# Kernel tuning notes

Measured on AMD Instinct MI355X. Metric: run time of the kernel, lower is better.

## Reference

```python
import jax, jax.numpy as jnp
import numpy as np

B, S, D = 1, 2048, 1024
E, F, TOP_K = 8, 2048, 2
LN_EPS = 1e-5


def setup_inputs() -> dict:
    key = jax.random.key(0)
    ks = jax.random.split(key, 8)
    sc_in = 1.0 / np.sqrt(D)
    sc_hid = 1.0 / np.sqrt(F)
    return {
        "x": jax.random.normal(ks[0], (B, S, D), dtype=jnp.float32),
        "Wr": jax.random.normal(ks[1], (D, E), dtype=jnp.float32) * sc_in,
        "br": jnp.zeros((E,), dtype=jnp.float32),
        "W1": jax.random.normal(ks[2], (E, D, F), dtype=jnp.float32) * sc_in,
        "b1": jnp.zeros((E, F), dtype=jnp.float32),
        "W2": jax.random.normal(ks[3], (E, F, D), dtype=jnp.float32) * sc_hid,
        "b2": jnp.zeros((E, D), dtype=jnp.float32),
        "gamma": jnp.ones((D,), dtype=jnp.float32),
        "beta": jnp.zeros((D,), dtype=jnp.float32),
    }


def reference(x, Wr, br, W1, b1, W2, b2, gamma, beta):
    # x: (B, S, D)
    xf = x.reshape(-1, D)  # (T, D), T = B*S
    # Router: softmax over expert logits, then top-k scores/indices.
    probs = jax.nn.softmax(xf @ Wr + br, axis=-1)           # (T, E)
    scores, idx = jax.lax.top_k(probs, TOP_K)               # (T, K)
    # combine[t, e] = sum_k scores[t, k] * [idx[t, k] == e]  (weighted scatter)
    onehot = jax.nn.one_hot(idx, E, dtype=xf.dtype)         # (T, K, E)
    combine = jnp.einsum('tk,tke->te', scores, onehot)      # (T, E)
    # Per-expert FFN, weighted scatter-add combine. Tokens not routed to an
    # expert have combine weight 0 -> identical math to masked gather/scatter.
    out = jnp.zeros_like(xf)
    for e in range(E):  # E is a small static constant
        h = jax.nn.gelu(xf @ W1[e] + b1[e])                 # (T, F)
        out = out + combine[:, e:e + 1] * (h @ W2[e] + b2[e])
    # Residual + LayerNorm (dropout = 0)
    y = x + out.reshape(B, S, D)
    mu = jnp.mean(y, axis=-1, keepdims=True)
    var = jnp.mean(jnp.square(y - mu), axis=-1, keepdims=True)
    return (y - mu) * jax.lax.rsqrt(var + LN_EPS) * gamma + beta
```

## Files before the change

### kernel.cpp

```cpp
#include <hip/hip_runtime.h>

#define T_TOK 2048
#define DDIM  1024
#define EEXP  8
#define FDIM  2048

typedef __attribute__((ext_vector_type(8))) short bf16x8;
typedef __attribute__((ext_vector_type(4))) float f32x4;
typedef __attribute__((ext_vector_type(4))) unsigned short u16x4;

__device__ __forceinline__ unsigned short f2bf(float f) {
  union { float f; unsigned int u; } v; v.f = f;
  unsigned int r = v.u + 0x7FFF + ((v.u >> 16) & 1);
  return (unsigned short)(r >> 16);
}
__device__ __forceinline__ float gelu_tanh(float x) {
  const float c = 0.7978845608028654f;
  float t = c * (x + 0.044715f * x * x * x);
  return 0.5f * x * (1.0f + tanhf(t));
}
__device__ __forceinline__ void gload_lds16(const void* g, void* lds) {
  __builtin_amdgcn_global_load_lds(
      (const __attribute__((address_space(1))) void*)g,
      (__attribute__((address_space(3))) void*)lds, 16, 0, 0);
}

__global__ __launch_bounds__(256)
void router_kernel(const float* __restrict__ x, const float* __restrict__ Wr,
                   const float* __restrict__ br, float* __restrict__ combine) {
  int t = blockIdx.x;
  int tid = threadIdx.x;
  float acc[EEXP];
#pragma unroll
  for (int e = 0; e < EEXP; ++e) acc[e] = 0.f;
  const float* xr = x + (size_t)t * DDIM;
  for (int d = tid; d < DDIM; d += 256) {
    float xv = xr[d];
    const float* w = Wr + d * EEXP;
#pragma unroll
    for (int e = 0; e < EEXP; ++e) acc[e] += xv * w[e];
  }
#pragma unroll
  for (int e = 0; e < EEXP; ++e)
    for (int off = 32; off > 0; off >>= 1) acc[e] += __shfl_down(acc[e], off);
  __shared__ float red[4][EEXP];
  int wave = tid >> 6, lane = tid & 63;
  if (lane == 0)
#pragma unroll
    for (int e = 0; e < EEXP; ++e) red[wave][e] = acc[e];
  __syncthreads();
  if (tid == 0) {
    float l[EEXP];
#pragma unroll
    for (int e = 0; e < EEXP; ++e)
      l[e] = red[0][e] + red[1][e] + red[2][e] + red[3][e] + br[e];
    int i0 = 0;
    for (int e = 1; e < EEXP; ++e) if (l[e] > l[i0]) i0 = e;
    int i1 = -1;
    for (int e = 0; e < EEXP; ++e) {
      if (e == i0) continue;
      if (i1 < 0 || l[e] > l[i1]) i1 = e;
    }
    float m = l[0];
    for (int e = 1; e < EEXP; ++e) m = fmaxf(m, l[e]);
    float p[EEXP], s = 0.f;
#pragma unroll
    for (int e = 0; e < EEXP; ++e) { p[e] = __expf(l[e] - m); s += p[e]; }
    float inv = 1.0f / s;
#pragma unroll
    for (int e = 0; e < EEXP; ++e)
      combine[t * EEXP + e] = (e == i0 || e == i1) ? p[e] * inv : 0.0f;
  }
}

__global__ __launch_bounds__(512)
void compact_kernel(const float* __restrict__ combine, int* __restrict__ idx,
                    int* __restrict__ meta) {
  int e = threadIdx.x >> 6, lane = threadIdx.x & 63;
  int cnt = 0;
  for (int t0 = 0; t0 < T_TOK; t0 += 64) {
    int t = t0 + lane;
    bool f = combine[t * EEXP + e] != 0.0f;
    unsigned long long m = __ballot(f);
    if (f) idx[e * T_TOK + cnt + __popcll(m & ((1ull << lane) - 1))] = t;
    cnt += __popcll(m);
  }
  __shared__ int sc[EEXP];
  if (lane == 0) sc[e] = cnt;
  __syncthreads();
  if (threadIdx.x == 0) {
    int b = 0;
    for (int i = 0; i < EEXP; ++i) { meta[i] = sc[i]; meta[8 + i] = b; b += sc[i]; }
    meta[16] = b;
  }
}

__global__ __launch_bounds__(256)
void wconv_kernel(const float* __restrict__ W1, const float* __restrict__ W2,
                  unsigned short* __restrict__ W1t, unsigned short* __restrict__ W2t) {
  __shared__ float tile[32][33];
  int z = blockIdx.z;
  const float* in; unsigned short* out; int R, C;
  if (z < 8) { in = W1 + (size_t)z * DDIM * FDIM; out = W1t + (size_t)z * DDIM * FDIM; R = DDIM; C = FDIM; }
  else       { in = W2 + (size_t)(z - 8) * DDIM * FDIM; out = W2t + (size_t)(z - 8) * DDIM * FDIM; R = FDIM; C = DDIM; }
  int tilesC = C >> 5;
  int tr = blockIdx.x / tilesC, tc = blockIdx.x % tilesC;
  int r0 = tr << 5, c0 = tc << 5;
  int t = threadIdx.x;
  int lr = t >> 3, lc4 = (t & 7) << 2;
  const float4 v = *(const float4*)(in + (size_t)(r0 + lr) * C + c0 + lc4);
  tile[lr][lc4 + 0] = v.x; tile[lr][lc4 + 1] = v.y;
  tile[lr][lc4 + 2] = v.z; tile[lr][lc4 + 3] = v.w;
  __syncthreads();
  u16x4 o;
  o[0] = f2bf(tile[lc4 + 0][lr]);
  o[1] = f2bf(tile[lc4 + 1][lr]);
  o[2] = f2bf(tile[lc4 + 2][lr]);
  o[3] = f2bf(tile[lc4 + 3][lr]);
  *(u16x4*)(out + (size_t)(c0 + lr) * R + r0 + lc4) = o;
}

__global__ __launch_bounds__(256)
void xconv_kernel(const float* __restrict__ x, unsigned short* __restrict__ xbf) {
  int i = blockIdx.x * 256 + threadIdx.x;
  const float4 v = *(const float4*)(x + (size_t)i * 4);
  u16x4 o; o[0] = f2bf(v.x); o[1] = f2bf(v.y); o[2] = f2bf(v.z); o[3] = f2bf(v.w);
  *(u16x4*)(xbf + (size_t)i * 4) = o;
}

template<int EPI>
__global__ __launch_bounds__(256)
void gemm_kernel(const unsigned short* __restrict__ A,
                 const unsigned short* __restrict__ Ball,
                 const float* __restrict__ ball,
                 const float* __restrict__ combine,
                 const int* __restrict__ idx,
                 const int* __restrict__ meta,
                 int K, int N,
                 unsigned short* __restrict__ Hc,
                 float* __restrict__ accum) {
  __shared__ unsigned short Asub[128 * 64];
  __shared__ unsigned short Bsub[128 * 64];
  int e = blockIdx.z;
  int cnt = meta[e];
  int m0 = blockIdx.y << 7;
  if (m0 >= cnt) return;
  int base = meta[8 + e];
  const unsigned short* B = Ball + (size_t)e * K * N;
  const float* bias = ball + (size_t)e * N;
  int n0 = blockIdx.x << 7;
  int tid = threadIdx.x, wave = tid >> 6, lane = tid & 63;
  int wm = wave >> 1, wn = wave & 1;
  int lr = lane & 15, lk = lane >> 4;

  int arow[4], brow[4], scol[4];
#pragma unroll
  for (int i = 0; i < 4; ++i) {
    int phys = i * 4096 + wave * 1024 + lane * 16;
    int row = phys >> 7;
    int lc = (phys & 127) ^ ((row & 7) << 4);
    scol[i] = lc >> 1;
    int lrow = min(m0 + row, cnt - 1);
    arow[i] = (EPI == 0) ? idx[e * T_TOK + lrow] : (base + lrow);
    brow[i] = n0 + row;
  }
  f32x4 acc[4][4] = {};

  for (int kt = 0; kt < K; kt += 64) {
#pragma unroll
    for (int i = 0; i < 4; ++i) {
      gload_lds16(A + (size_t)arow[i] * K + kt + scol[i],
                  (char*)Asub + i * 4096 + wave * 1024);
      gload_lds16(B + (size_t)brow[i] * K + kt + scol[i],
                  (char*)Bsub + i * 4096 + wave * 1024);
    }
    __syncthreads();
#pragma unroll
    for (int ks = 0; ks < 2; ++ks) {
      bf16x8 af[4], bf_[4];
#pragma unroll
      for (int m = 0; m < 4; ++m) {
        int row = wm * 64 + m * 16 + lr;
        int cb = (ks * 64 + lk * 16) ^ ((row & 7) << 4);
        af[m] = *(const bf16x8*)((const char*)Asub + row * 128 + cb);
      }
#pragma unroll
      for (int n = 0; n < 4; ++n) {
        int row = wn * 64 + n * 16 + lr;
        int cb = (ks * 64 + lk * 16) ^ ((row & 7) << 4);
        bf_[n] = *(const bf16x8*)((const char*)Bsub + row * 128 + cb);
      }
#pragma unroll
      for (int m = 0; m < 4; ++m)
#pragma unroll
        for (int n = 0; n < 4; ++n)
          acc[m][n] = __builtin_amdgcn_mfma_f32_16x16x32_bf16(af[m], bf_[n], acc[m][n], 0, 0, 0);
    }
    __syncthreads();
  }

  if (EPI == 0) {
#pragma unroll
    for (int m = 0; m < 4; ++m) {
      int lbase = m0 + wm * 64 + m * 16 + lk * 4;
#pragma unroll
      for (int n = 0; n < 4; ++n) {
        int col = n0 + wn * 64 + n * 16 + lr;
        float bv = bias[col];
#pragma unroll
        for (int r = 0; r < 4; ++r) {
          int local = lbase + r;
          if (local < cnt)
            Hc[(size_t)(base + local) * N + col] = f2bf(gelu_tanh(acc[m][n][r] + bv));
        }
      }
    }
  } else {
#pragma unroll
    for (int m = 0; m < 4; ++m) {
      int lbase = m0 + wm * 64 + m * 16 + lk * 4;
#pragma unroll
      for (int r = 0; r < 4; ++r) {
        int local = lbase + r;
        if (local < cnt) {
          int tok = idx[e * T_TOK + local];
          float c = combine[tok * EEXP + e];
#pragma unroll
          for (int n = 0; n < 4; ++n) {
            int col = n0 + wn * 64 + n * 16 + lr;
            atomicAdd(&accum[(size_t)tok * N + col], c * (acc[m][n][r] + bias[col]));
          }
        }
      }
    }
  }
}

__global__ __launch_bounds__(256)
void ln_kernel(const float* __restrict__ x, const float* __restrict__ accum,
               const float* __restrict__ gamma, const float* __restrict__ beta,
               float* __restrict__ out) {
  int r = blockIdx.x, tid = threadIdx.x;
  size_t base = (size_t)r * DDIM + tid * 4;
  float4 xv = *(const float4*)(x + base);
  float4 av = *(const float4*)(accum + base);
  float y[4] = { xv.x + av.x, xv.y + av.y, xv.z + av.z, xv.w + av.w };
  float s = y[0] + y[1] + y[2] + y[3];
  float s2 = y[0] * y[0] + y[1] * y[1] + y[2] * y[2] + y[3] * y[3];
  for (int off = 32; off > 0; off >>= 1) {
    s += __shfl_down(s, off);
    s2 += __shfl_down(s2, off);
  }
  __shared__ float rs[4], rs2[4];
  int wave = tid >> 6, lane = tid & 63;
  if (lane == 0) { rs[wave] = s; rs2[wave] = s2; }
  __syncthreads();
  float ts = rs[0] + rs[1] + rs[2] + rs[3];
  float ts2 = rs2[0] + rs2[1] + rs2[2] + rs2[3];
  float mu = ts * (1.0f / DDIM);
  float var = ts2 * (1.0f / DDIM) - mu * mu;
  float inv = rsqrtf(var + 1e-5f);
  float4 gv = *(const float4*)(gamma + tid * 4);
  float4 bv = *(const float4*)(beta + tid * 4);
  float4 o;
  o.x = (y[0] - mu) * inv * gv.x + bv.x;
  o.y = (y[1] - mu) * inv * gv.y + bv.y;
  o.z = (y[2] - mu) * inv * gv.z + bv.z;
  o.w = (y[3] - mu) * inv * gv.w + bv.w;
  *(float4*)(out + base) = o;
}

#define BM 128
#define BN 128
#define BK 32
#define LDT 40

__global__ __launch_bounds__(256)
void g1_old(const float* __restrict__ X, const float* __restrict__ W1,
            const float* __restrict__ b1, unsigned short* __restrict__ H) {
  __shared__ unsigned short As[BM][LDT];
  __shared__ unsigned short Bs[BN][LDT];
  int tid = threadIdx.x;
  int trow0 = blockIdx.y * BM, ncol0 = blockIdx.x * BN;
  int wave = tid >> 6, lane = tid & 63;
  int wm = wave >> 1, wn = wave & 1;
  int lr = lane & 15, lk = lane >> 4;
  f32x4 acc[4][4] = {};
  for (int kt = 0; kt < DDIM; kt += BK) {
#pragma unroll
    for (int it = 0; it < 4; ++it) {
      int i = tid + it * 256;
      int row = i >> 3, c4 = (i & 7) << 2;
      const float4 v = *(const float4*)(X + (size_t)(trow0 + row) * DDIM + kt + c4);
      uint2 p;
      p.x = (unsigned int)f2bf(v.x) | ((unsigned int)f2bf(v.y) << 16);
      p.y = (unsigned int)f2bf(v.z) | ((unsigned int)f2bf(v.w) << 16);
      *(uint2*)&As[row][c4] = p;
    }
#pragma unroll
    for (int it = 0; it < 4; ++it) {
      int i = tid + it * 256;
      int r = i >> 5, c4 = (i & 31) << 2;
      const float4 v = *(const float4*)(W1 + (size_t)(kt + r) * FDIM + ncol0 + c4);
      Bs[c4 + 0][r] = f2bf(v.x); Bs[c4 + 1][r] = f2bf(v.y);
      Bs[c4 + 2][r] = f2bf(v.z); Bs[c4 + 3][r] = f2bf(v.w);
    }
    __syncthreads();
    bf16x8 af[4], bfr[4];
#pragma unroll
    for (int m = 0; m < 4; ++m) af[m] = *(const bf16x8*)&As[wm * 64 + m * 16 + lr][lk * 8];
#pragma unroll
    for (int n = 0; n < 4; ++n) bfr[n] = *(const bf16x8*)&Bs[wn * 64 + n * 16 + lr][lk * 8];
#pragma unroll
    for (int m = 0; m < 4; ++m)
#pragma unroll
      for (int n = 0; n < 4; ++n)
        acc[m][n] = __builtin_amdgcn_mfma_f32_16x16x32_bf16(af[m], bfr[n], acc[m][n], 0, 0, 0);
    __syncthreads();
  }
#pragma unroll
  for (int m = 0; m < 4; ++m) {
    int row = trow0 + wm * 64 + m * 16 + lk * 4;
#pragma unroll
    for (int n = 0; n < 4; ++n) {
      int col = ncol0 + wn * 64 + n * 16 + lr;
      float bv = b1[col];
#pragma unroll
      for (int r = 0; r < 4; ++r)
        H[(size_t)(row + r) * FDIM + col] = f2bf(gelu_tanh(acc[m][n][r] + bv));
    }
  }
}

__global__ __launch_bounds__(256)
void g2_old(const unsigned short* __restrict__ H, const float* __restrict__ W2,
            const float* __restrict__ b2, const float* __restrict__ combine,
            int e, float* __restrict__ out) {
  __shared__ unsigned short As[BM][LDT];
  __shared__ unsigned short Bs[BN][LDT];
  int tid = threadIdx.x;
  int trow0 = blockIdx.y * BM, ncol0 = blockIdx.x * BN;
  int wave = tid >> 6, lane = tid & 63;
  int wm = wave >> 1, wn = wave & 1;
  int lr = lane & 15, lk = lane >> 4;
  f32x4 acc[4][4] = {};
  for (int kt = 0; kt < FDIM; kt += BK) {
#pragma unroll
    for (int it = 0; it < 2; ++it) {
      int i = tid + it * 256;
      int row = i >> 2, c8 = (i & 3) << 3;
      uint4 v = *(const uint4*)(H + (size_t)(trow0 + row) * FDIM + kt + c8);
      *(uint4*)&As[row][c8] = v;
    }
#pragma unroll
    for (int it = 0; it < 4; ++it) {
      int i = tid + it * 256;
      int r = i >> 5, c4 = (i & 31) << 2;
      const float4 v = *(const float4*)(W2 + (size_t)(kt + r) * DDIM + ncol0 + c4);
      Bs[c4 + 0][r] = f2bf(v.x); Bs[c4 + 1][r] = f2bf(v.y);
      Bs[c4 + 2][r] = f2bf(v.z); Bs[c4 + 3][r] = f2bf(v.w);
    }
    __syncthreads();
    bf16x8 af[4], bfr[4];
#pragma unroll
    for (int m = 0; m < 4; ++m) af[m] = *(const bf16x8*)&As[wm * 64 + m * 16 + lr][lk * 8];
#pragma unroll
    for (int n = 0; n < 4; ++n) bfr[n] = *(const bf16x8*)&Bs[wn * 64 + n * 16 + lr][lk * 8];
#pragma unroll
    for (int m = 0; m < 4; ++m)
#pragma unroll
      for (int n = 0; n < 4; ++n)
        acc[m][n] = __builtin_amdgcn_mfma_f32_16x16x32_bf16(af[m], bfr[n], acc[m][n], 0, 0, 0);
    __syncthreads();
  }
#pragma unroll
  for (int m = 0; m < 4; ++m) {
    int row = trow0 + wm * 64 + m * 16 + lk * 4;
#pragma unroll
    for (int n = 0; n < 4; ++n) {
      int col = ncol0 + wn * 64 + n * 16 + lr;
      float bv = b2[col];
#pragma unroll
      for (int r = 0; r < 4; ++r) {
        int rr = row + r;
        float c = combine[rr * EEXP + e];
        if (c != 0.0f) out[(size_t)rr * DDIM + col] += c * (acc[m][n][r] + bv);
      }
    }
  }
}

extern "C" void kernel_launch(void* const* d_in, const int* in_sizes, int n_in,
                              void* d_out, int out_size, void* d_ws, size_t ws_size,
                              hipStream_t stream) {
  const float* x     = (const float*)d_in[0];
  const float* Wr    = (const float*)d_in[1];
  const float* br    = (const float*)d_in[2];
  const float* W1    = (const float*)d_in[3];
  const float* b1    = (const float*)d_in[4];
  const float* W2    = (const float*)d_in[5];
  const float* b2    = (const float*)d_in[6];
  const float* gamma = (const float*)d_in[7];
  const float* beta  = (const float*)d_in[8];

  size_t off_combine = 0;
  size_t off_meta    = off_combine + (size_t)T_TOK * EEXP * 4;
  size_t off_idx     = off_meta + 1024;
  size_t off_xbf     = off_idx + (size_t)EEXP * T_TOK * 4;
  size_t off_accum   = off_xbf + (size_t)T_TOK * DDIM * 2;
  size_t off_Hc      = off_accum + (size_t)T_TOK * DDIM * 4;
  size_t off_W1t     = off_Hc + (size_t)2 * T_TOK * FDIM * 2;
  size_t off_W2t     = off_W1t + (size_t)EEXP * DDIM * FDIM * 2;
  size_t need        = off_W2t + (size_t)EEXP * DDIM * FDIM * 2;

  float* combine = (float*)((char*)d_ws + off_combine);

  if (ws_size >= need) {
    int*   meta  = (int*)((char*)d_ws + off_meta);
    int*   idx   = (int*)((char*)d_ws + off_idx);
    unsigned short* xbf = (unsigned short*)((char*)d_ws + off_xbf);
    float* accum = (float*)((char*)d_ws + off_accum);
    unsigned short* Hc  = (unsigned short*)((char*)d_ws + off_Hc);
    unsigned short* W1t = (unsigned short*)((char*)d_ws + off_W1t);
    unsigned short* W2t = (unsigned short*)((char*)d_ws + off_W2t);

    wconv_kernel<<<dim3(2048, 1, 16), 256, 0, stream>>>(W1, W2, W1t, W2t);
    xconv_kernel<<<(T_TOK * DDIM / 4) / 256, 256, 0, stream>>>(x, xbf);
    router_kernel<<<T_TOK, 256, 0, stream>>>(x, Wr, br, combine);
    compact_kernel<<<1, 512, 0, stream>>>(combine, idx, meta);
    hipMemsetAsync(accum, 0, (size_t)T_TOK * DDIM * 4, stream);
    gemm_kernel<0><<<dim3(FDIM / 128, T_TOK / 128, EEXP), 256, 0, stream>>>(
        xbf, W1t, b1, combine, idx, meta, DDIM, FDIM, Hc, nullptr);
    gemm_kernel<1><<<dim3(DDIM / 128, T_TOK / 128, EEXP), 256, 0, stream>>>(
        Hc, W2t, b2, combine, idx, meta, FDIM, DDIM, nullptr, accum);
    ln_kernel<<<T_TOK, 256, 0, stream>>>(x, accum, gamma, beta, (float*)d_out);
  } else {
    float* accum = (float*)((char*)d_ws + off_xbf);
    unsigned short* Hbf = (unsigned short*)(accum + (size_t)T_TOK * DDIM);
    hipMemsetAsync(accum, 0, (size_t)T_TOK * DDIM * 4, stream);
    router_kernel<<<T_TOK, 256, 0, stream>>>(x, Wr, br, combine);
    for (int e = 0; e < EEXP; ++e) {
      g1_old<<<dim3(FDIM / BN, T_TOK / BM), 256, 0, stream>>>(
          x, W1 + (size_t)e * DDIM * FDIM, b1 + (size_t)e * FDIM, Hbf);
      g2_old<<<dim3(DDIM / BN, T_TOK / BM), 256, 0, stream>>>(
          Hbf, W2 + (size_t)e * FDIM * DDIM, b2 + (size_t)e * DDIM, combine, e, accum);
    }
    ln_kernel<<<T_TOK, 256, 0, stream>>>(x, accum, gamma, beta, (float*)d_out);
  }
}
```

Measured before the change: 324.2 us.

## Double-buffer MoE GEMM LDS, split-K second GEMM, remap grid, fuse x conversion

The expert GEMMs now use two LDS buffers, so the next K-tile is loaded while MFMAs run on the current one. The grid becomes a 1D launch with a custom block-to-(expert, m-tile, n-tile) mapping. The second GEMM is split in K across two halves, giving more blocks and adding bias only once, at the cost of doubling atomic adds to the accumulator. The fp32-to-bf16 conversion of x is folded into the router kernel to remove one launch; the fallback path passes a scratch buffer for it.

```diff
diff --git a/kernel.cpp b/kernel.cpp
--- a/kernel.cpp
+++ b/kernel.cpp
@@ -27,15 +27,18 @@
 
 __global__ __launch_bounds__(256)
 void router_kernel(const float* __restrict__ x, const float* __restrict__ Wr,
-                   const float* __restrict__ br, float* __restrict__ combine) {
+                   const float* __restrict__ br, float* __restrict__ combine,
+                   unsigned short* __restrict__ xbf) {
   int t = blockIdx.x;
   int tid = threadIdx.x;
   float acc[EEXP];
 #pragma unroll
   for (int e = 0; e < EEXP; ++e) acc[e] = 0.f;
   const float* xr = x + (size_t)t * DDIM;
+  unsigned short* xbr = xbf + (size_t)t * DDIM;
   for (int d = tid; d < DDIM; d += 256) {
     float xv = xr[d];
+    xbr[d] = f2bf(xv);
     const float* w = Wr + d * EEXP;
 #pragma unroll
     for (int e = 0; e < EEXP; ++e) acc[e] += xv * w[e];
@@ -120,14 +123,6 @@
   *(u16x4*)(out + (size_t)(c0 + lr) * R + r0 + lc4) = o;
 }
 
-__global__ __launch_bounds__(256)
-void xconv_kernel(const float* __restrict__ x, unsigned short* __restrict__ xbf) {
-  int i = blockIdx.x * 256 + threadIdx.x;
-  const float4 v = *(const float4*)(x + (size_t)i * 4);
-  u16x4 o; o[0] = f2bf(v.x); o[1] = f2bf(v.y); o[2] = f2bf(v.z); o[3] = f2bf(v.w);
-  *(u16x4*)(xbf + (size_t)i * 4) = o;
-}
-
 template<int EPI>
 __global__ __launch_bounds__(256)
 void gemm_kernel(const unsigned short* __restrict__ A,
@@ -136,19 +131,30 @@
                  const float* __restrict__ combine,
                  const int* __restrict__ idx,
                  const int* __restrict__ meta,
-                 int K, int N,
                  unsigned short* __restrict__ Hc,
                  float* __restrict__ accum) {
-  __shared__ unsigned short Asub[128 * 64];
-  __shared__ unsigned short Bsub[128 * 64];
-  int e = blockIdx.z;
+  constexpr int KF = (EPI == 0) ? DDIM : FDIM;
+  constexpr int N  = (EPI == 0) ? FDIM : DDIM;
+  constexpr int NT = 16;
+  __shared__ unsigned short Asub[2 * 128 * 64];
+  __shared__ unsigned short Bsub[2 * 128 * 64];
+
+  int id = blockIdx.x;
+  int a = id >> 7, rem = id & 127;
+  int mtile = rem >> 3, b = rem & 7;
+  int ne = a * 8 + b;
+  int nsl = ne & 15, e = ne >> 4;
+  int ntile, kbeg;
+  if (EPI == 0) { ntile = nsl; kbeg = 0; }
+  else          { ntile = nsl & 7; kbeg = (nsl >> 3) * 1024; }
+
   int cnt = meta[e];
-  int m0 = blockIdx.y << 7;
+  int m0 = mtile << 7;
   if (m0 >= cnt) return;
   int base = meta[8 + e];
-  const unsigned short* B = Ball + (size_t)e * K * N;
+  const unsigned short* B = Ball + (size_t)e * KF * N;
   const float* bias = ball + (size_t)e * N;
-  int n0 = blockIdx.x << 7;
+  int n0 = ntile << 7;
   int tid = threadIdx.x, wave = tid >> 6, lane = tid & 63;
   int wm = wave >> 1, wn = wave & 1;
   int lr = lane & 15, lk = lane >> 4;
@@ -164,17 +170,23 @@
     arow[i] = (EPI == 0) ? idx[e * T_TOK + lrow] : (base + lrow);
     brow[i] = n0 + row;
   }
+
+  auto stage = [&](int buf, int kt) {
+#pragma unroll
+    for (int i = 0; i < 4; ++i) {
+      gload_lds16(A + (size_t)arow[i] * KF + kt + scol[i],
+                  (char*)Asub + buf * 16384 + i * 4096 + wave * 1024);
+      gload_lds16(B + (size_t)brow[i] * KF + kt + scol[i],
+                  (char*)Bsub + buf * 16384 + i * 4096 + wave * 1024);
+    }
+  };
+
   f32x4 acc[4][4] = {};
-
-  for (int kt = 0; kt < K; kt += 64) {
-#pragma unroll
-    for (int i = 0; i < 4; ++i) {
-      gload_lds16(A + (size_t)arow[i] * K + kt + scol[i],
-                  (char*)Asub + i * 4096 + wave * 1024);
-      gload_lds16(B + (size_t)brow[i] * K + kt + scol[i],
-                  (char*)Bsub + i * 4096 + wave * 1024);
-    }
-    __syncthreads();
+  stage(0, kbeg);
+  __syncthreads();
+  int cur = 0;
+  for (int t = 0; t < NT; ++t) {
+    if (t + 1 < NT) stage(cur ^ 1, kbeg + (t + 1) * 64);
 #pragma unroll
     for (int ks = 0; ks < 2; ++ks) {
       bf16x8 af[4], bf_[4];
@@ -182,13 +194,13 @@
       for (int m = 0; m < 4; ++m) {
         int row = wm * 64 + m * 16 + lr;
         int cb = (ks * 64 + lk * 16) ^ ((row & 7) << 4);
-        af[m] = *(const bf16x8*)((const char*)Asub + row * 128 + cb);
+        af[m] = *(const bf16x8*)((const char*)Asub + cur * 16384 + row * 128 + cb);
       }
 #pragma unroll
       for (int n = 0; n < 4; ++n) {
         int row = wn * 64 + n * 16 + lr;
         int cb = (ks * 64 + lk * 16) ^ ((row & 7) << 4);
-        bf_[n] = *(const bf16x8*)((const char*)Bsub + row * 128 + cb);
+        bf_[n] = *(const bf16x8*)((const char*)Bsub + cur * 16384 + row * 128 + cb);
       }
 #pragma unroll
       for (int m = 0; m < 4; ++m)
@@ -197,6 +209,7 @@
           acc[m][n] = __builtin_amdgcn_mfma_f32_16x16x32_bf16(af[m], bf_[n], acc[m][n], 0, 0, 0);
     }
     __syncthreads();
+    cur ^= 1;
   }
 
   if (EPI == 0) {
@@ -216,6 +229,7 @@
       }
     }
   } else {
+    bool addb = (kbeg == 0);
 #pragma unroll
     for (int m = 0; m < 4; ++m) {
       int lbase = m0 + wm * 64 + m * 16 + lk * 4;
@@ -228,7 +242,8 @@
 #pragma unroll
           for (int n = 0; n < 4; ++n) {
             int col = n0 + wn * 64 + n * 16 + lr;
-            atomicAdd(&accum[(size_t)tok * N + col], c * (acc[m][n][r] + bias[col]));
+            float v = acc[m][n][r] + (addb ? bias[col] : 0.0f);
+            atomicAdd(&accum[(size_t)tok * N + col], c * v);
           }
         }
       }
@@ -425,20 +440,17 @@
     unsigned short* W2t = (unsigned short*)((char*)d_ws + off_W2t);
 
     wconv_kernel<<<dim3(2048, 1, 16), 256, 0, stream>>>(W1, W2, W1t, W2t);
-    xconv_kernel<<<(T_TOK * DDIM / 4) / 256, 256, 0, stream>>>(x, xbf);
-    router_kernel<<<T_TOK, 256, 0, stream>>>(x, Wr, br, combine);
+    router_kernel<<<T_TOK, 256, 0, stream>>>(x, Wr, br, combine, xbf);
     compact_kernel<<<1, 512, 0, stream>>>(combine, idx, meta);
     hipMemsetAsync(accum, 0, (size_t)T_TOK * DDIM * 4, stream);
-    gemm_kernel<0><<<dim3(FDIM / 128, T_TOK / 128, EEXP), 256, 0, stream>>>(
-        xbf, W1t, b1, combine, idx, meta, DDIM, FDIM, Hc, nullptr);
-    gemm_kernel<1><<<dim3(DDIM / 128, T_TOK / 128, EEXP), 256, 0, stream>>>(
-        Hc, W2t, b2, combine, idx, meta, FDIM, DDIM, nullptr, accum);
+    gemm_kernel<0><<<2048, 256, 0, stream>>>(xbf, W1t, b1, combine, idx, meta, Hc, nullptr);
+    gemm_kernel<1><<<2048, 256, 0, stream>>>(Hc, W2t, b2, combine, idx, meta, nullptr, accum);
     ln_kernel<<<T_TOK, 256, 0, stream>>>(x, accum, gamma, beta, (float*)d_out);
   } else {
     float* accum = (float*)((char*)d_ws + off_xbf);
     unsigned short* Hbf = (unsigned short*)(accum + (size_t)T_TOK * DDIM);
     hipMemsetAsync(accum, 0, (size_t)T_TOK * DDIM * 4, stream);
-    router_kernel<<<T_TOK, 256, 0, stream>>>(x, Wr, br, combine);
+    router_kernel<<<T_TOK, 256, 0, stream>>>(x, Wr, br, combine, Hbf );
     for (int e = 0; e < EEXP; ++e) {
       g1_old<<<dim3(FDIM / BN, T_TOK / BM), 256, 0, stream>>>(
           x, W1 + (size_t)e * DDIM * FDIM, b1 + (size_t)e * FDIM, Hbf);
```

Measured after the change: 355.6 us. 1.1x slower.
